# Kernel tuning notes

Hardware: AMD Instinct MI355X
Metric: run time of the kernel (lower is better)

Reference implementation:

```python
import jax, jax.numpy as jnp
import numpy as np

FH = FW = 3

def _decomp_layer(x, f0, f1, f2, f3):
    # x: (B, C, H, W); f0: (F, r), f1: (FH, r), f2: (FW, r), f3: (C, r)
    B, C, H, W = x.shape
    Ho, Wo = H - FH + 1, W - FW + 1
    # unfold -> patches (B, C, Ho, Wo, FH, FW); fixed 3x3 loop, not a data-dim loop
    patches = jnp.stack(
        [jnp.stack([x[:, :, i:i + Ho, j:j + Wo] for j in range(FW)], axis=-1)
         for i in range(FH)], axis=-2)
    # permute to (B, Ho, Wo, FH, FW, C) as in torch's permute(0,2,3,4,5,1)
    patches = patches.transpose(0, 2, 3, 4, 5, 1)
    # CP contraction: collapse fh, fw, c against rank factors, then expand to filters
    t = jnp.einsum('bhwxyc,xr,yr,cr->bhwr', patches, f1, f2, f3)
    return jnp.einsum('bhwr,fr->bfhw', t, f0)  # (B, F, Ho, Wo)


def setup_inputs() -> dict:
    key = jax.random.key(0)
    ks = jax.random.split(key, 12)
    B, C, H, W = 512, 3, 32, 32
    F, R, NC = 32, 16, 10
    s = 0.1
    return {
        'x': jax.random.normal(ks[0], (B, C, H, W), jnp.float32),
        'l1_f0': jax.random.normal(ks[1], (F, R), jnp.float32) * s,
        'l1_f1': jax.random.normal(ks[2], (FH, R), jnp.float32) * s,
        'l1_f2': jax.random.normal(ks[3], (FW, R), jnp.float32) * s,
        'l1_f3': jax.random.normal(ks[4], (C, R), jnp.float32) * s,
        'l2_f0': jax.random.normal(ks[5], (F, R), jnp.float32) * s,
        'l2_f1': jax.random.normal(ks[6], (FH, R), jnp.float32) * s,
        'l2_f2': jax.random.normal(ks[7], (FW, R), jnp.float32) * s,
        'l2_f3': jax.random.normal(ks[8], (F, R), jnp.float32) * s,
        'W_cls': jax.random.normal(ks[9], (NC, 25088), jnp.float32) * 0.01,
        'b_cls': jnp.zeros((NC,), jnp.float32),
    }


def reference(x, l1_f0, l1_f1, l1_f2, l1_f3, l2_f0, l2_f1, l2_f2, l2_f3, W_cls, b_cls):
    h = _decomp_layer(x, l1_f0, l1_f1, l1_f2, l1_f3)        # (B, 32, 30, 30)
    h = _decomp_layer(h, l2_f0, l2_f1, l2_f2, l2_f3)        # (B, 32, 28, 28)
    h = h.reshape(h.shape[0], -1)                            # (B, 25088)
    logits = h @ W_cls.T + b_cls
    return jax.nn.log_softmax(logits, axis=1)
```

## Files before the change

### kernel.cpp

```cpp
#include <hip/hip_runtime.h>
#include <math.h>


#define NT 512

__global__ void precomp_kernel(const float* __restrict__ l1_f0,
                               const float* __restrict__ l2_f0,
                               const float* __restrict__ l2_f3,
                               const float* __restrict__ Wcls,
                               float* __restrict__ Wc2,
                               float* __restrict__ Mm,
                               float* __restrict__ Lg) {
    int id = blockIdx.x * blockDim.x + threadIdx.x;
    if (id < 7840) {
        int n = id / 784;
        int pix = id - n * 784;
        const float* wrow = &Wcls[n * 25088 + pix];
        float acc[16];
#pragma unroll
        for (int r2 = 0; r2 < 16; ++r2) acc[r2] = 0.f;
#pragma unroll
        for (int f = 0; f < 32; ++f) {
            float wv = wrow[f * 784];
#pragma unroll
            for (int r2 = 0; r2 < 16; ++r2)
                acc[r2] += l2_f0[f * 16 + r2] * wv;
        }
#pragma unroll
        for (int r2 = 0; r2 < 16; ++r2)
            Wc2[(n * 16 + r2) * 784 + pix] = acc[r2];
    }
    if (id < 256) {
        int r1 = id >> 4, r2 = id & 15;
        float acc = 0.f;
#pragma unroll
        for (int f = 0; f < 32; ++f)
            acc += l1_f0[f * 16 + r1] * l2_f3[f * 16 + r2];
        Mm[id] = acc;
    }
    if (id < 5120) Lg[id] = 0.f;
}

__global__ __launch_bounds__(NT, 4) void fused_half_kernel(
    const float* __restrict__ x,
    const float* __restrict__ l1_f1, const float* __restrict__ l1_f2,
    const float* __restrict__ l1_f3,
    const float* __restrict__ l2_f1, const float* __restrict__ l2_f2,
    const float* __restrict__ Wc2, const float* __restrict__ Mm,
    float* __restrict__ Lg) {
    __shared__ alignas(16) float sA[16 * 576];
    __shared__ alignas(16) float sB[16 * 480];
    __shared__ float sw1[144];
    __shared__ float sw2[144];
    __shared__ alignas(16) float sM[256];
    __shared__ float sred[8 * 10];

    const int tid = threadIdx.x;
    const int b = blockIdx.x >> 1;
    const int h = blockIdx.x & 1;
    const int r0s = h * 14;

    if (tid < 144) {
        int r = tid / 9, ij = tid - r * 9;
        int i = ij / 3, j = ij - i * 3;
        sw1[tid] = l1_f1[i * 16 + r] * l1_f2[j * 16 + r];
    }
    if (tid >= 144 && tid < 288) {
        int t = tid - 144;
        int r = t / 9, ij = t - r * 9;
        int i = ij / 3, j = ij - i * 3;
        sw2[t] = l2_f1[i * 16 + r] * l2_f2[j * 16 + r];
    }
    if (tid < 256) sM[tid] = Mm[tid];

    {
        const int xbase = b * 3072 + r0s * 32;
        {
            const int p = tid;
            float x0 = x[xbase + p];
            float x1 = x[xbase + 1024 + p];
            float x2 = x[xbase + 2048 + p];
#pragma unroll
            for (int r = 0; r < 16; ++r)
                sA[r * 576 + p] = x0 * l1_f3[r] + x1 * l1_f3[16 + r] + x2 * l1_f3[32 + r];
        }
        if (tid < 64) {
            const int p = 512 + tid;
            float x0 = x[xbase + p];
            float x1 = x[xbase + 1024 + p];
            float x2 = x[xbase + 2048 + p];
#pragma unroll
            for (int r = 0; r < 16; ++r)
                sA[r * 576 + p] = x0 * l1_f3[r] + x1 * l1_f3[16 + r] + x2 * l1_f3[32 + r];
        }
    }
    __syncthreads();

    if (tid < 480) {
        const int r = tid / 30;
        const int t = tid - r * 30;
        const int q = t / 15;
        const int pr = t - q * 15;
        const int c = 2 * pr;
        const int row0 = q * 8;
        const float* wp = &sw1[r * 9];
        const float w0 = wp[0], w1 = wp[1], w2 = wp[2];
        const float w3 = wp[3], w4 = wp[4], w5 = wp[5];
        const float w6 = wp[6], w7 = wp[7], w8 = wp[8];
        const float* base = &sA[r * 576 + row0 * 32 + c];
        float2 aL = *(const float2*)&base[0];
        float2 aH = *(const float2*)&base[2];
        float2 bL = *(const float2*)&base[32];
        float2 bH = *(const float2*)&base[34];
        float a0 = aL.x, a1 = aL.y, a2 = aH.x, a3 = aH.y;
        float b0 = bL.x, b1 = bL.y, b2 = bH.x, b3 = bH.y;
        float* op = &sB[r * 480 + row0 * 30 + c];
#pragma unroll
        for (int s = 0; s < 8; ++s) {
            const float* rp = base + (s + 2) * 32;
            float2 cL = *(const float2*)&rp[0];
            float2 cH = *(const float2*)&rp[2];
            float c0 = cL.x, c1 = cL.y, c2 = cH.x, c3 = cH.y;
            float o0 = w0 * a0 + w1 * a1 + w2 * a2
                     + w3 * b0 + w4 * b1 + w5 * b2
                     + w6 * c0 + w7 * c1 + w8 * c2;
            float o1 = w0 * a1 + w1 * a2 + w2 * a3
                     + w3 * b1 + w4 * b2 + w5 * b3
                     + w6 * c1 + w7 * c2 + w8 * c3;
            *(float2*)&op[s * 30] = make_float2(o0, o1);
            a0 = b0; a1 = b1; a2 = b2; a3 = b3;
            b0 = c0; b1 = c1; b2 = c2; b3 = c3;
        }
    }
    __syncthreads();

    if (tid < 480) {
        const int tr = tid & 3;
        const int tp = tid >> 2;
        const int p4 = tp * 4;
        const int r2b = tr * 4;
        float a00 = 0.f, a01 = 0.f, a02 = 0.f, a03 = 0.f;
        float a10 = 0.f, a11 = 0.f, a12 = 0.f, a13 = 0.f;
        float a20 = 0.f, a21 = 0.f, a22 = 0.f, a23 = 0.f;
        float a30 = 0.f, a31 = 0.f, a32 = 0.f, a33 = 0.f;
#pragma unroll
        for (int r1 = 0; r1 < 16; ++r1) {
            float4 tv = *(const float4*)&sB[r1 * 480 + p4];
            float4 mv = *(const float4*)&sM[r1 * 16 + r2b];
            a00 += mv.x * tv.x; a01 += mv.x * tv.y; a02 += mv.x * tv.z; a03 += mv.x * tv.w;
            a10 += mv.y * tv.x; a11 += mv.y * tv.y; a12 += mv.y * tv.z; a13 += mv.y * tv.w;
            a20 += mv.z * tv.x; a21 += mv.z * tv.y; a22 += mv.z * tv.z; a23 += mv.z * tv.w;
            a30 += mv.w * tv.x; a31 += mv.w * tv.y; a32 += mv.w * tv.z; a33 += mv.w * tv.w;
        }
        *(float4*)&sA[(r2b + 0) * 480 + p4] = make_float4(a00, a01, a02, a03);
        *(float4*)&sA[(r2b + 1) * 480 + p4] = make_float4(a10, a11, a12, a13);
        *(float4*)&sA[(r2b + 2) * 480 + p4] = make_float4(a20, a21, a22, a23);
        *(float4*)&sA[(r2b + 3) * 480 + p4] = make_float4(a30, a31, a32, a33);
    }
    __syncthreads();

    if (tid < 448) {
        const int r2 = tid / 28;
        const int t = tid - r2 * 28;
        const int q = t / 14;
        const int pr = t - q * 14;
        const int c = 2 * pr;
        const int row0 = q * 7;
        const float* wp = &sw2[r2 * 9];
        const float w0 = wp[0], w1 = wp[1], w2 = wp[2];
        const float w3 = wp[3], w4 = wp[4], w5 = wp[5];
        const float w6 = wp[6], w7 = wp[7], w8 = wp[8];
        const float* base = &sA[r2 * 480 + row0 * 30 + c];
        float2 aL = *(const float2*)&base[0];
        float2 aH = *(const float2*)&base[2];
        float2 bL = *(const float2*)&base[30];
        float2 bH = *(const float2*)&base[32];
        float a0 = aL.x, a1 = aL.y, a2 = aH.x, a3 = aH.y;
        float b0 = bL.x, b1 = bL.y, b2 = bH.x, b3 = bH.y;
        float* op = &sB[r2 * 392 + row0 * 28 + c];
#pragma unroll
        for (int s = 0; s < 7; ++s) {
            const float* rp = base + (s + 2) * 30;
            float2 cL = *(const float2*)&rp[0];
            float2 cH = *(const float2*)&rp[2];
            float c0 = cL.x, c1 = cL.y, c2 = cH.x, c3 = cH.y;
            float o0 = w0 * a0 + w1 * a1 + w2 * a2
                     + w3 * b0 + w4 * b1 + w5 * b2
                     + w6 * c0 + w7 * c1 + w8 * c2;
            float o1 = w0 * a1 + w1 * a2 + w2 * a3
                     + w3 * b1 + w4 * b2 + w5 * b3
                     + w6 * c1 + w7 * c2 + w8 * c3;
            *(float2*)&op[s * 28] = make_float2(o0, o1);
            a0 = b0; a1 = b1; a2 = b2; a3 = b3;
            b0 = c0; b1 = c1; b2 = c2; b3 = c3;
        }
    }
    __syncthreads();

    float acc[10];
#pragma unroll
    for (int n = 0; n < 10; ++n) acc[n] = 0.f;
    const int hoff = h * 392;
    for (int k = tid; k < 1568; k += NT) {
        const int r2 = k / 98;
        const int rem = k - r2 * 98;
        float4 tv = *(const float4*)&sB[k * 4];
        const float* wp = &Wc2[r2 * 784 + hoff + rem * 4];
#pragma unroll
        for (int n = 0; n < 10; ++n) {
            float4 wv = *(const float4*)&wp[n * 12544];
            acc[n] += tv.x * wv.x + tv.y * wv.y + tv.z * wv.z + tv.w * wv.w;
        }
    }
#pragma unroll
    for (int n = 0; n < 10; ++n) {
        float v = acc[n];
#pragma unroll
        for (int off = 32; off > 0; off >>= 1)
            v += __shfl_down(v, off, 64);
        if ((tid & 63) == 0) sred[(tid >> 6) * 10 + n] = v;
    }
    __syncthreads();
    if (tid < 10) {
        float lg = 0.f;
#pragma unroll
        for (int w = 0; w < 8; ++w) lg += sred[w * 10 + tid];
        atomicAdd(&Lg[b * 10 + tid], lg);
    }
}

__global__ void logsoftmax_kernel(const float* __restrict__ Lg,
                                  const float* __restrict__ b_cls,
                                  float* __restrict__ out) {
    int b = blockIdx.x * blockDim.x + threadIdx.x;
    if (b < 512) {
        float v[10];
        float m = -1e30f;
#pragma unroll
        for (int n = 0; n < 10; ++n) {
            v[n] = Lg[b * 10 + n] + b_cls[n];
            m = fmaxf(m, v[n]);
        }
        float s = 0.f;
#pragma unroll
        for (int n = 0; n < 10; ++n) s += expf(v[n] - m);
        float lse = m + logf(s);
#pragma unroll
        for (int n = 0; n < 10; ++n) out[b * 10 + n] = v[n] - lse;
    }
}

extern "C" void kernel_launch(void* const* d_in, const int* in_sizes, int n_in,
                              void* d_out, int out_size, void* d_ws, size_t ws_size,
                              hipStream_t stream) {
    const float* x     = (const float*)d_in[0];
    const float* l1_f0 = (const float*)d_in[1];
    const float* l1_f1 = (const float*)d_in[2];
    const float* l1_f2 = (const float*)d_in[3];
    const float* l1_f3 = (const float*)d_in[4];
    const float* l2_f0 = (const float*)d_in[5];
    const float* l2_f1 = (const float*)d_in[6];
    const float* l2_f2 = (const float*)d_in[7];
    const float* l2_f3 = (const float*)d_in[8];
    const float* Wcls  = (const float*)d_in[9];
    const float* bcls  = (const float*)d_in[10];
    float* out = (float*)d_out;

    float* Wc2 = (float*)d_ws;
    float* Mm  = Wc2 + 10 * 16 * 784;
    float* Lg  = Mm + 256;

    precomp_kernel<<<dim3(31), dim3(256), 0, stream>>>(
        l1_f0, l2_f0, l2_f3, Wcls, Wc2, Mm, Lg);
    fused_half_kernel<<<dim3(1024), dim3(NT), 0, stream>>>(
        x, l1_f1, l1_f2, l1_f3, l2_f1, l2_f2, Wc2, Mm, Lg);
    logsoftmax_kernel<<<dim3(2), dim3(256), 0, stream>>>(Lg, bcls, out);
}
```

Measured before the change: 111.2 us.

## Fuse log-softmax via last-block counter and double threads per block

The log-softmax kernel is folded into the main kernel. A per-sample atomic counter lets the second of the two half-image blocks finish the softmax, which removes a kernel launch. The block grows to 1024 threads, and each conv and rank-mixing stage is split into finer per-thread work. The prologue loads run in parallel across thread ranges, and the first-stage shared buffer gets a padded row stride. The classifier weights are re-laid out per half so each block reads one contiguous slice, making the final dot product a straight-line loop. The cost is threadfence and atomic overhead plus tighter register limits from the higher occupancy bound.

Result: slower. 129.0 us (+16.0%).

```diff
diff --git a/kernel.cpp b/kernel.cpp
--- a/kernel.cpp
+++ b/kernel.cpp
@@ -2,19 +2,25 @@
 #include <math.h>
 
 
-#define NT 512
+#define NT 1024
+#define S1S 34
 
 __global__ void precomp_kernel(const float* __restrict__ l1_f0,
                                const float* __restrict__ l2_f0,
                                const float* __restrict__ l2_f3,
                                const float* __restrict__ Wcls,
-                               float* __restrict__ Wc2,
+                               float* __restrict__ Wc2L,
                                float* __restrict__ Mm,
-                               float* __restrict__ Lg) {
+                               float* __restrict__ Lg,
+                               unsigned int* __restrict__ Cnt) {
     int id = blockIdx.x * blockDim.x + threadIdx.x;
     if (id < 7840) {
         int n = id / 784;
         int pix = id - n * 784;
+        int row = pix / 28;
+        int col = pix - row * 28;
+        int h = (row < 14) ? 0 : 1;
+        int lr = row - h * 14;
         const float* wrow = &Wcls[n * 25088 + pix];
         float acc[16];
 #pragma unroll
@@ -26,9 +32,10 @@
             for (int r2 = 0; r2 < 16; ++r2)
                 acc[r2] += l2_f0[f * 16 + r2] * wv;
         }
+        float* dst = &Wc2L[n * 12544 + h * 6272 + lr * 28 + col];
 #pragma unroll
         for (int r2 = 0; r2 < 16; ++r2)
-            Wc2[(n * 16 + r2) * 784 + pix] = acc[r2];
+            dst[r2 * 392] = acc[r2];
     }
     if (id < 256) {
         int r1 = id >> 4, r2 = id & 15;
@@ -39,133 +46,130 @@
         Mm[id] = acc;
     }
     if (id < 5120) Lg[id] = 0.f;
+    if (id >= 5120 && id < 5632) Cnt[id - 5120] = 0u;
 }
 
-__global__ __launch_bounds__(NT, 4) void fused_half_kernel(
+__global__ __launch_bounds__(NT, 8) void fused_half_kernel(
     const float* __restrict__ x,
     const float* __restrict__ l1_f1, const float* __restrict__ l1_f2,
     const float* __restrict__ l1_f3,
     const float* __restrict__ l2_f1, const float* __restrict__ l2_f2,
-    const float* __restrict__ Wc2, const float* __restrict__ Mm,
-    float* __restrict__ Lg) {
-    __shared__ alignas(16) float sA[16 * 576];
+    const float* __restrict__ Wc2L, const float* __restrict__ Mm,
+    const float* __restrict__ b_cls,
+    float* __restrict__ Lg, unsigned int* __restrict__ Cnt,
+    float* __restrict__ out) {
+    __shared__ alignas(16) float sA[16 * 18 * S1S];
     __shared__ alignas(16) float sB[16 * 480];
     __shared__ float sw1[144];
     __shared__ float sw2[144];
     __shared__ alignas(16) float sM[256];
-    __shared__ float sred[8 * 10];
+    __shared__ float sred[16 * 10];
+    __shared__ float slog[10];
+    __shared__ int sflag;
 
     const int tid = threadIdx.x;
     const int b = blockIdx.x >> 1;
     const int h = blockIdx.x & 1;
-    const int r0s = h * 14;
 
     if (tid < 144) {
         int r = tid / 9, ij = tid - r * 9;
         int i = ij / 3, j = ij - i * 3;
         sw1[tid] = l1_f1[i * 16 + r] * l1_f2[j * 16 + r];
-    }
-    if (tid >= 144 && tid < 288) {
+    } else if (tid < 288) {
         int t = tid - 144;
         int r = t / 9, ij = t - r * 9;
         int i = ij / 3, j = ij - i * 3;
         sw2[t] = l2_f1[i * 16 + r] * l2_f2[j * 16 + r];
-    }
-    if (tid < 256) sM[tid] = Mm[tid];
-
-    {
-        const int xbase = b * 3072 + r0s * 32;
-        {
-            const int p = tid;
-            float x0 = x[xbase + p];
-            float x1 = x[xbase + 1024 + p];
-            float x2 = x[xbase + 2048 + p];
-#pragma unroll
-            for (int r = 0; r < 16; ++r)
-                sA[r * 576 + p] = x0 * l1_f3[r] + x1 * l1_f3[16 + r] + x2 * l1_f3[32 + r];
-        }
-        if (tid < 64) {
-            const int p = 512 + tid;
-            float x0 = x[xbase + p];
-            float x1 = x[xbase + 1024 + p];
-            float x2 = x[xbase + 2048 + p];
-#pragma unroll
-            for (int r = 0; r < 16; ++r)
-                sA[r * 576 + p] = x0 * l1_f3[r] + x1 * l1_f3[16 + r] + x2 * l1_f3[32 + r];
-        }
-    }
-    __syncthreads();
-
-    if (tid < 480) {
-        const int r = tid / 30;
-        const int t = tid - r * 30;
+    } else if (tid < 544) {
+        sM[tid - 288] = Mm[tid - 288];
+    } else if (tid < 832) {
+        const int p = (tid - 544) * 2;
+        const int row = p >> 5, col = p & 31;
+        const int xbase = b * 3072 + h * 14 * 32 + p;
+        float2 x0 = *(const float2*)&x[xbase];
+        float2 x1 = *(const float2*)&x[xbase + 1024];
+        float2 x2 = *(const float2*)&x[xbase + 2048];
+        const int o = row * S1S + col;
+#pragma unroll
+        for (int r = 0; r < 16; ++r) {
+            float f0 = l1_f3[r], f1 = l1_f3[16 + r], f2 = l1_f3[32 + r];
+            *(float2*)&sA[r * (18 * S1S) + o] =
+                make_float2(x0.x * f0 + x1.x * f1 + x2.x * f2,
+                            x0.y * f0 + x1.y * f1 + x2.y * f2);
+        }
+    }
+    __syncthreads();
+
+    if (tid < 960) {
+        const int r = tid / 60;
+        const int t = tid - r * 60;
         const int q = t / 15;
         const int pr = t - q * 15;
         const int c = 2 * pr;
-        const int row0 = q * 8;
+        const int row0 = q * 4;
         const float* wp = &sw1[r * 9];
         const float w0 = wp[0], w1 = wp[1], w2 = wp[2];
         const float w3 = wp[3], w4 = wp[4], w5 = wp[5];
         const float w6 = wp[6], w7 = wp[7], w8 = wp[8];
-        const float* base = &sA[r * 576 + row0 * 32 + c];
+        const float* base = &sA[r * (18 * S1S) + row0 * S1S + c];
         float2 aL = *(const float2*)&base[0];
         float2 aH = *(const float2*)&base[2];
-        float2 bL = *(const float2*)&base[32];
-        float2 bH = *(const float2*)&base[34];
+        float2 bL = *(const float2*)&base[S1S];
+        float2 bH = *(const float2*)&base[S1S + 2];
         float a0 = aL.x, a1 = aL.y, a2 = aH.x, a3 = aH.y;
         float b0 = bL.x, b1 = bL.y, b2 = bH.x, b3 = bH.y;
         float* op = &sB[r * 480 + row0 * 30 + c];
 #pragma unroll
-        for (int s = 0; s < 8; ++s) {
-            const float* rp = base + (s + 2) * 32;
+        for (int s = 0; s < 4; ++s) {
+            const float* rp = base + (s + 2) * S1S;
             float2 cL = *(const float2*)&rp[0];
             float2 cH = *(const float2*)&rp[2];
-            float c0 = cL.x, c1 = cL.y, c2 = cH.x, c3 = cH.y;
             float o0 = w0 * a0 + w1 * a1 + w2 * a2
                      + w3 * b0 + w4 * b1 + w5 * b2
-                     + w6 * c0 + w7 * c1 + w8 * c2;
+                     + w6 * cL.x + w7 * cL.y + w8 * cH.x;
             float o1 = w0 * a1 + w1 * a2 + w2 * a3
                      + w3 * b1 + w4 * b2 + w5 * b3
-                     + w6 * c1 + w7 * c2 + w8 * c3;
+                     + w6 * cL.y + w7 * cH.x + w8 * cH.y;
             *(float2*)&op[s * 30] = make_float2(o0, o1);
             a0 = b0; a1 = b1; a2 = b2; a3 = b3;
-            b0 = c0; b1 = c1; b2 = c2; b3 = c3;
-        }
-    }
-    __syncthreads();
-
-    if (tid < 480) {
+            b0 = cL.x; b1 = cL.y; b2 = cH.x; b3 = cH.y;
+        }
+    }
+    __syncthreads();
+
+    if (tid < 960) {
         const int tr = tid & 3;
         const int tp = tid >> 2;
-        const int p4 = tp * 4;
+        const int p2 = tp * 2;
         const int r2b = tr * 4;
-        float a00 = 0.f, a01 = 0.f, a02 = 0.f, a03 = 0.f;
-        float a10 = 0.f, a11 = 0.f, a12 = 0.f, a13 = 0.f;
-        float a20 = 0.f, a21 = 0.f, a22 = 0.f, a23 = 0.f;
-        float a30 = 0.f, a31 = 0.f, a32 = 0.f, a33 = 0.f;
+        float a00 = 0.f, a01 = 0.f;
+        float a10 = 0.f, a11 = 0.f;
+        float a20 = 0.f, a21 = 0.f;
+        float a30 = 0.f, a31 = 0.f;
 #pragma unroll
         for (int r1 = 0; r1 < 16; ++r1) {
-            float4 tv = *(const float4*)&sB[r1 * 480 + p4];
+            float2 tv = *(const float2*)&sB[r1 * 480 + p2];
             float4 mv = *(const float4*)&sM[r1 * 16 + r2b];
-            a00 += mv.x * tv.x; a01 += mv.x * tv.y; a02 += mv.x * tv.z; a03 += mv.x * tv.w;
-            a10 += mv.y * tv.x; a11 += mv.y * tv.y; a12 += mv.y * tv.z; a13 += mv.y * tv.w;
-            a20 += mv.z * tv.x; a21 += mv.z * tv.y; a22 += mv.z * tv.z; a23 += mv.z * tv.w;
-            a30 += mv.w * tv.x; a31 += mv.w * tv.y; a32 += mv.w * tv.z; a33 += mv.w * tv.w;
-        }
-        *(float4*)&sA[(r2b + 0) * 480 + p4] = make_float4(a00, a01, a02, a03);
-        *(float4*)&sA[(r2b + 1) * 480 + p4] = make_float4(a10, a11, a12, a13);
-        *(float4*)&sA[(r2b + 2) * 480 + p4] = make_float4(a20, a21, a22, a23);
-        *(float4*)&sA[(r2b + 3) * 480 + p4] = make_float4(a30, a31, a32, a33);
-    }
-    __syncthreads();
-
-    if (tid < 448) {
-        const int r2 = tid / 28;
-        const int t = tid - r2 * 28;
+            a00 += mv.x * tv.x; a01 += mv.x * tv.y;
+            a10 += mv.y * tv.x; a11 += mv.y * tv.y;
+            a20 += mv.z * tv.x; a21 += mv.z * tv.y;
+            a30 += mv.w * tv.x; a31 += mv.w * tv.y;
+        }
+        *(float2*)&sA[(r2b + 0) * 480 + p2] = make_float2(a00, a01);
+        *(float2*)&sA[(r2b + 1) * 480 + p2] = make_float2(a10, a11);
+        *(float2*)&sA[(r2b + 2) * 480 + p2] = make_float2(a20, a21);
+        *(float2*)&sA[(r2b + 3) * 480 + p2] = make_float2(a30, a31);
+    }
+    __syncthreads();
+
+    if (tid < 896) {
+        const int r2 = tid / 56;
+        const int t = tid - r2 * 56;
         const int q = t / 14;
         const int pr = t - q * 14;
         const int c = 2 * pr;
-        const int row0 = q * 7;
+        const int row0 = (q < 2) ? q * 4 : (8 + 3 * (q - 2));
+        const int nrows = (q < 2) ? 4 : 3;
         const float* wp = &sw2[r2 * 9];
         const float w0 = wp[0], w1 = wp[1], w2 = wp[2];
         const float w3 = wp[3], w4 = wp[4], w5 = wp[5];
@@ -179,20 +183,21 @@
         float b0 = bL.x, b1 = bL.y, b2 = bH.x, b3 = bH.y;
         float* op = &sB[r2 * 392 + row0 * 28 + c];
 #pragma unroll
-        for (int s = 0; s < 7; ++s) {
-            const float* rp = base + (s + 2) * 30;
-            float2 cL = *(const float2*)&rp[0];
-            float2 cH = *(const float2*)&rp[2];
-            float c0 = cL.x, c1 = cL.y, c2 = cH.x, c3 = cH.y;
-            float o0 = w0 * a0 + w1 * a1 + w2 * a2
-                     + w3 * b0 + w4 * b1 + w5 * b2
-                     + w6 * c0 + w7 * c1 + w8 * c2;
-            float o1 = w0 * a1 + w1 * a2 + w2 * a3
-                     + w3 * b1 + w4 * b2 + w5 * b3
-                     + w6 * c1 + w7 * c2 + w8 * c3;
-            *(float2*)&op[s * 28] = make_float2(o0, o1);
-            a0 = b0; a1 = b1; a2 = b2; a3 = b3;
-            b0 = c0; b1 = c1; b2 = c2; b3 = c3;
+        for (int s = 0; s < 4; ++s) {
+            if (s < nrows) {
+                const float* rp = base + (s + 2) * 30;
+                float2 cL = *(const float2*)&rp[0];
+                float2 cH = *(const float2*)&rp[2];
+                float o0 = w0 * a0 + w1 * a1 + w2 * a2
+                         + w3 * b0 + w4 * b1 + w5 * b2
+                         + w6 * cL.x + w7 * cL.y + w8 * cH.x;
+                float o1 = w0 * a1 + w1 * a2 + w2 * a3
+                         + w3 * b1 + w4 * b2 + w5 * b3
+                         + w6 * cL.y + w7 * cH.x + w8 * cH.y;
+                *(float2*)&op[s * 28] = make_float2(o0, o1);
+                a0 = b0; a1 = b1; a2 = b2; a3 = b3;
+                b0 = cL.x; b1 = cL.y; b2 = cH.x; b3 = cH.y;
+            }
         }
     }
     __syncthreads();
@@ -200,16 +205,22 @@
     float acc[10];
 #pragma unroll
     for (int n = 0; n < 10; ++n) acc[n] = 0.f;
-    const int hoff = h * 392;
-    for (int k = tid; k < 1568; k += NT) {
-        const int r2 = k / 98;
-        const int rem = k - r2 * 98;
-        float4 tv = *(const float4*)&sB[k * 4];
-        const float* wp = &Wc2[r2 * 784 + hoff + rem * 4];
+    const float* wbase = &Wc2L[h * 6272];
+    {
+        float4 tv = *(const float4*)&sB[tid * 4];
 #pragma unroll
         for (int n = 0; n < 10; ++n) {
-            float4 wv = *(const float4*)&wp[n * 12544];
+            float4 wv = *(const float4*)&wbase[n * 12544 + tid * 4];
             acc[n] += tv.x * wv.x + tv.y * wv.y + tv.z * wv.z + tv.w * wv.w;
+        }
+        if (tid < 544) {
+            const int k = tid + 1024;
+            float4 tv2 = *(const float4*)&sB[k * 4];
+#pragma unroll
+            for (int n = 0; n < 10; ++n) {
+                float4 wv = *(const float4*)&wbase[n * 12544 + k * 4];
+                acc[n] += tv2.x * wv.x + tv2.y * wv.y + tv2.z * wv.z + tv2.w * wv.w;
+            }
         }
     }
 #pragma unroll
@@ -224,29 +235,30 @@
     if (tid < 10) {
         float lg = 0.f;
 #pragma unroll
-        for (int w = 0; w < 8; ++w) lg += sred[w * 10 + tid];
+        for (int w = 0; w < 16; ++w) lg += sred[w * 10 + tid];
         atomicAdd(&Lg[b * 10 + tid], lg);
     }
-}
-
-__global__ void logsoftmax_kernel(const float* __restrict__ Lg,
-                                  const float* __restrict__ b_cls,
-                                  float* __restrict__ out) {
-    int b = blockIdx.x * blockDim.x + threadIdx.x;
-    if (b < 512) {
-        float v[10];
-        float m = -1e30f;
-#pragma unroll
-        for (int n = 0; n < 10; ++n) {
-            v[n] = Lg[b * 10 + n] + b_cls[n];
-            m = fmaxf(m, v[n]);
-        }
-        float s = 0.f;
-#pragma unroll
-        for (int n = 0; n < 10; ++n) s += expf(v[n] - m);
-        float lse = m + logf(s);
-#pragma unroll
-        for (int n = 0; n < 10; ++n) out[b * 10 + n] = v[n] - lse;
+    if (tid == 0) {
+        __threadfence();
+        unsigned int old = atomicAdd(&Cnt[b], 1u);
+        sflag = (old == 1u) ? 1 : 0;
+    }
+    __syncthreads();
+    if (sflag) {
+        if (tid < 10) {
+            float v = atomicAdd(&Lg[b * 10 + tid], 0.0f) + b_cls[tid];
+            slog[tid] = v;
+        }
+        __syncthreads();
+        if (tid < 10) {
+            float m = -1e30f;
+#pragma unroll
+            for (int n = 0; n < 10; ++n) m = fmaxf(m, slog[n]);
+            float s = 0.f;
+#pragma unroll
+            for (int n = 0; n < 10; ++n) s += expf(slog[n] - m);
+            out[b * 10 + tid] = slog[tid] - m - logf(s);
+        }
     }
 }
 
@@ -266,13 +278,13 @@
     const float* bcls  = (const float*)d_in[10];
     float* out = (float*)d_out;
 
-    float* Wc2 = (float*)d_ws;
-    float* Mm  = Wc2 + 10 * 16 * 784;
-    float* Lg  = Mm + 256;
+    float* Wc2L = (float*)d_ws;
+    float* Mm   = Wc2L + 10 * 12544;
+    float* Lg   = Mm + 256;
+    unsigned int* Cnt = (unsigned int*)(Lg + 5120);
 
     precomp_kernel<<<dim3(31), dim3(256), 0, stream>>>(
-        l1_f0, l2_f0, l2_f3, Wcls, Wc2, Mm, Lg);
+        l1_f0, l2_f0, l2_f3, Wcls, Wc2L, Mm, Lg, Cnt);
     fused_half_kernel<<<dim3(1024), dim3(NT), 0, stream>>>(
-        x, l1_f1, l1_f2, l1_f3, l2_f1, l2_f2, Wc2, Mm, Lg);
-    logsoftmax_kernel<<<dim3(2), dim3(256), 0, stream>>>(Lg, bcls, out);
+        x, l1_f1, l1_f2, l1_f3, l2_f1, l2_f2, Wc2L, Mm, bcls, Lg, Cnt, out);
 }
```
